# Optimization experiments

Measured on AMD Instinct MI355X. Metric: run time of the kernel, lower is better.

## Reference

```python
import jax, jax.numpy as jnp
import numpy as np

THRESHOLD = 0.95
SECONDARY = 0.5


def setup_inputs() -> dict:
    key = jax.random.key(0)
    quantum_states = jax.random.normal(key, (8, 2048, 64), dtype=jnp.float32)
    return {"quantum_states": quantum_states}


def reference(quantum_states):
    # quantum_states: (B, N, D)
    B, N, D = quantum_states.shape
    # pairwise fidelity: (states @ states^T)^2 -> (B, N, N)
    dots = jnp.einsum("bnd,bmd->bnm", quantum_states, quantum_states)
    fid = dots * dots
    # edge weights: 1.0 if fid >= threshold, else SECONDARY if fid >= secondary, else 0
    w = jnp.where(fid >= THRESHOLD, jnp.float32(1.0),
                  jnp.where(fid >= SECONDARY, jnp.float32(SECONDARY), jnp.float32(0.0)))
    # zero out diagonal (only i < j pairs form edges)
    eye = jnp.eye(N, dtype=bool)
    w = jnp.where(eye[None, :, :], jnp.float32(0.0), w)
    # Laplacian L = D - W
    deg = jnp.sum(w, axis=-1)  # (B, N)
    lap = -w
    idx = jnp.arange(N)
    lap = lap.at[:, idx, idx].set(deg)
    return lap
```

## Files before the change

kernel.cpp:

```cpp
#include <hip/hip_runtime.h>

typedef __attribute__((ext_vector_type(8))) __bf16 bf16x8;
typedef __attribute__((ext_vector_type(4))) __bf16 bf16x4;
typedef __attribute__((ext_vector_type(4))) float f32x4;

#define LDST 72

__device__ __forceinline__ void lds_barrier() {
    asm volatile("s_waitcnt lgkmcnt(0)" ::: "memory");
    __builtin_amdgcn_s_barrier();
    __builtin_amdgcn_sched_barrier(0);
}
__device__ __forceinline__ void full_barrier() {
    asm volatile("s_waitcnt vmcnt(0) lgkmcnt(0)" ::: "memory");
    __builtin_amdgcn_s_barrier();
    __builtin_amdgcn_sched_barrier(0);
}

__global__ __launch_bounds__(512) void lap_strip_kernel(
    const float* __restrict__ X, float* __restrict__ out, int N)
{
    const int flat   = blockIdx.x;
    const int b      = flat & 7;
    const int strip0 = (flat >> 3) * 32;
    const int tid  = threadIdx.x;
    const int lane = tid & 63;
    const int w    = tid >> 6;
    const int t    = lane & 15;
    const int g    = lane >> 4;

    __shared__ __align__(16) unsigned short As[2][128 * LDST];
    __shared__ __align__(16) unsigned short Bs[32 * LDST];
    __shared__ float deg_part[8][32];

    const float* Xb   = X   + (size_t)b * N * 64;
    float*       outb = out + (size_t)b * N * N;

    {
        const float4* src = reinterpret_cast<const float4*>(Xb + (size_t)strip0 * 64);
        int r = tid >> 4, q = tid & 15;
        float4 v = src[tid];
        bf16x4 h = {(__bf16)v.x, (__bf16)v.y, (__bf16)v.z, (__bf16)v.w};
        *reinterpret_cast<bf16x4*>(&Bs[r * LDST + q * 4]) = h;
    }

    float4 pre[4];
    {
        const float4* src = reinterpret_cast<const float4*>(Xb);
#pragma unroll
        for (int it = 0; it < 4; ++it) pre[it] = src[tid + it * 512];
#pragma unroll
        for (int it = 0; it < 4; ++it) {
            int idx = tid + it * 512;
            int r = idx >> 4, q = idx & 15;
            float4 v = pre[it];
            bf16x4 h = {(__bf16)v.x, (__bf16)v.y, (__bf16)v.z, (__bf16)v.w};
            *reinterpret_cast<bf16x4*>(&As[0][r * LDST + q * 4]) = h;
        }
    }
    lds_barrier();

    bf16x8 bfrag[2][2];
#pragma unroll
    for (int ks = 0; ks < 2; ++ks)
#pragma unroll
        for (int fj = 0; fj < 2; ++fj)
            bfrag[ks][fj] = *reinterpret_cast<const bf16x8*>(
                &Bs[(16 * fj + t) * LDST + ks * 32 + g * 8]);

    float rs[2] = {0.f, 0.f};
    int cur = 0;
    const int nct = N >> 7;
    const int diag_ct = strip0 >> 7;

    for (int ct = 0; ct < nct; ++ct) {
        if (ct + 1 < nct) {
            const float4* src = reinterpret_cast<const float4*>(Xb + (size_t)(ct + 1) * 128 * 64);
#pragma unroll
            for (int it = 0; it < 4; ++it) pre[it] = src[tid + it * 512];
        }

        f32x4 acc[2] = {};
#pragma unroll
        for (int ks = 0; ks < 2; ++ks) {
            const int koff = ks * 32 + g * 8;
            bf16x8 a = *reinterpret_cast<const bf16x8*>(
                &As[cur][(16 * w + t) * LDST + koff]);
#pragma unroll
            for (int fj = 0; fj < 2; ++fj)
                acc[fj] = __builtin_amdgcn_mfma_f32_16x16x32_bf16(
                    a, bfrag[ks][fj], acc[fj], 0, 0, 0);
        }

        const bool has_diag = (ct == diag_ct);
#pragma unroll
        for (int fj = 0; fj < 2; ++fj) {
            const int orow  = strip0 + 16 * fj + t;
            const int ocol0 = ct * 128 + 16 * w + 4 * g;
            float wv[4];
#pragma unroll
            for (int r = 0; r < 4; ++r) {
                const float d = acc[fj][r];
                float wt = (fabsf(d) >= 0.97467943f) ? 1.0f
                         : ((fabsf(d) >= 0.70710678f) ? 0.5f : 0.0f);
                if (has_diag && (ocol0 + r == orow)) wt = 0.0f;
                rs[fj] += wt;
                wv[r] = -wt;
            }
            f32x4 st = {wv[0], wv[1], wv[2], wv[3]};
            *reinterpret_cast<f32x4*>(&outb[(size_t)orow * N + ocol0]) = st;
        }

        if (ct + 1 < nct) {
#pragma unroll
            for (int it = 0; it < 4; ++it) {
                int idx = tid + it * 512;
                int r = idx >> 4, q = idx & 15;
                float4 v = pre[it];
                bf16x4 h = {(__bf16)v.x, (__bf16)v.y, (__bf16)v.z, (__bf16)v.w};
                *reinterpret_cast<bf16x4*>(&As[cur ^ 1][r * LDST + q * 4]) = h;
            }
        }
        lds_barrier();
        cur ^= 1;
    }

    rs[0] += __shfl_xor(rs[0], 16, 64); rs[0] += __shfl_xor(rs[0], 32, 64);
    rs[1] += __shfl_xor(rs[1], 16, 64); rs[1] += __shfl_xor(rs[1], 32, 64);
    if (g == 0) { deg_part[w][t] = rs[0]; deg_part[w][16 + t] = rs[1]; }
    full_barrier();
    if (tid < 32) {
        float d = 0.f;
#pragma unroll
        for (int ww = 0; ww < 8; ++ww) d += deg_part[ww][tid];
        const int rr = strip0 + tid;
        outb[(size_t)rr * N + rr] = d;
    }
}

extern "C" void kernel_launch(void* const* d_in, const int* in_sizes, int n_in,
                              void* d_out, int out_size, void* d_ws, size_t ws_size,
                              hipStream_t stream) {
    const float* X = (const float*)d_in[0];
    float* out = (float*)d_out;

    const int B = 8;
    const int D = 64;
    const int N = in_sizes[0] / (B * D);

    dim3 grid((N / 32) * B);
    lap_strip_kernel<<<grid, dim3(512), 0, stream>>>(X, out, N);
}
```

Baseline: 34.69 us.

## Stage weight codes in LDS and emit coalesced full-row stores per half

Result: slower. 35.67 us (+2.8%).

```diff
diff --git a/kernel.cpp b/kernel.cpp
--- a/kernel.cpp
+++ b/kernel.cpp
@@ -4,7 +4,11 @@
 typedef __attribute__((ext_vector_type(4))) __bf16 bf16x4;
 typedef __attribute__((ext_vector_type(4))) float f32x4;
 
-#define LDST 72
+#define LDST 68
+#define SROW 1032
+
+#define T_HI 0.97467943f
+#define T_LO 0.70710678f
 
 __device__ __forceinline__ void lds_barrier() {
     asm volatile("s_waitcnt lgkmcnt(0)" ::: "memory");
@@ -17,7 +21,7 @@
     __builtin_amdgcn_sched_barrier(0);
 }
 
-__global__ __launch_bounds__(512) void lap_strip_kernel(
+__global__ __launch_bounds__(512) void lap_stage_kernel(
     const float* __restrict__ X, float* __restrict__ out, int N)
 {
     const int flat   = blockIdx.x;
@@ -29,8 +33,9 @@
     const int t    = lane & 15;
     const int g    = lane >> 4;
 
-    __shared__ __align__(16) unsigned short As[2][128 * LDST];
+    __shared__ __align__(16) unsigned short As[128 * LDST];
     __shared__ __align__(16) unsigned short Bs[32 * LDST];
+    __shared__ __align__(4)  unsigned char  St[32 * SROW];
     __shared__ float deg_part[8][32];
 
     const float* Xb   = X   + (size_t)b * N * 64;
@@ -43,20 +48,11 @@
         bf16x4 h = {(__bf16)v.x, (__bf16)v.y, (__bf16)v.z, (__bf16)v.w};
         *reinterpret_cast<bf16x4*>(&Bs[r * LDST + q * 4]) = h;
     }
-
     float4 pre[4];
     {
         const float4* src = reinterpret_cast<const float4*>(Xb);
 #pragma unroll
         for (int it = 0; it < 4; ++it) pre[it] = src[tid + it * 512];
-#pragma unroll
-        for (int it = 0; it < 4; ++it) {
-            int idx = tid + it * 512;
-            int r = idx >> 4, q = idx & 15;
-            float4 v = pre[it];
-            bf16x4 h = {(__bf16)v.x, (__bf16)v.y, (__bf16)v.z, (__bf16)v.w};
-            *reinterpret_cast<bf16x4*>(&As[0][r * LDST + q * 4]) = h;
-        }
     }
     lds_barrier();
 
@@ -69,60 +65,79 @@
                 &Bs[(16 * fj + t) * LDST + ks * 32 + g * 8]);
 
     float rs[2] = {0.f, 0.f};
-    int cur = 0;
-    const int nct = N >> 7;
-    const int diag_ct = strip0 >> 7;
 
-    for (int ct = 0; ct < nct; ++ct) {
-        if (ct + 1 < nct) {
-            const float4* src = reinterpret_cast<const float4*>(Xb + (size_t)(ct + 1) * 128 * 64);
-#pragma unroll
-            for (int it = 0; it < 4; ++it) pre[it] = src[tid + it * 512];
-        }
+    for (int half = 0; half < 2; ++half) {
+#pragma unroll 1
+        for (int ctl = 0; ctl < 8; ++ctl) {
+            const int ct = half * 8 + ctl;
 
-        f32x4 acc[2] = {};
-#pragma unroll
-        for (int ks = 0; ks < 2; ++ks) {
-            const int koff = ks * 32 + g * 8;
-            bf16x8 a = *reinterpret_cast<const bf16x8*>(
-                &As[cur][(16 * w + t) * LDST + koff]);
-#pragma unroll
-            for (int fj = 0; fj < 2; ++fj)
-                acc[fj] = __builtin_amdgcn_mfma_f32_16x16x32_bf16(
-                    a, bfrag[ks][fj], acc[fj], 0, 0, 0);
-        }
-
-        const bool has_diag = (ct == diag_ct);
-#pragma unroll
-        for (int fj = 0; fj < 2; ++fj) {
-            const int orow  = strip0 + 16 * fj + t;
-            const int ocol0 = ct * 128 + 16 * w + 4 * g;
-            float wv[4];
-#pragma unroll
-            for (int r = 0; r < 4; ++r) {
-                const float d = acc[fj][r];
-                float wt = (fabsf(d) >= 0.97467943f) ? 1.0f
-                         : ((fabsf(d) >= 0.70710678f) ? 0.5f : 0.0f);
-                if (has_diag && (ocol0 + r == orow)) wt = 0.0f;
-                rs[fj] += wt;
-                wv[r] = -wt;
-            }
-            f32x4 st = {wv[0], wv[1], wv[2], wv[3]};
-            *reinterpret_cast<f32x4*>(&outb[(size_t)orow * N + ocol0]) = st;
-        }
-
-        if (ct + 1 < nct) {
 #pragma unroll
             for (int it = 0; it < 4; ++it) {
                 int idx = tid + it * 512;
                 int r = idx >> 4, q = idx & 15;
                 float4 v = pre[it];
                 bf16x4 h = {(__bf16)v.x, (__bf16)v.y, (__bf16)v.z, (__bf16)v.w};
-                *reinterpret_cast<bf16x4*>(&As[cur ^ 1][r * LDST + q * 4]) = h;
+                *reinterpret_cast<bf16x4*>(&As[r * LDST + q * 4]) = h;
+            }
+            lds_barrier();
+
+            if (ct + 1 < 16) {
+                const float4* src = reinterpret_cast<const float4*>(
+                    Xb + (size_t)(ct + 1) * 128 * 64);
+#pragma unroll
+                for (int it = 0; it < 4; ++it) pre[it] = src[tid + it * 512];
+            }
+
+            f32x4 acc[2] = {};
+#pragma unroll
+            for (int ks = 0; ks < 2; ++ks) {
+                const int koff = ks * 32 + g * 8;
+                bf16x8 a = *reinterpret_cast<const bf16x8*>(
+                    &As[(16 * w + t) * LDST + koff]);
+#pragma unroll
+                for (int fj = 0; fj < 2; ++fj)
+                    acc[fj] = __builtin_amdgcn_mfma_f32_16x16x32_bf16(
+                        a, bfrag[ks][fj], acc[fj], 0, 0, 0);
+            }
+
+            const int scol0 = 128 * ctl + 16 * w + 4 * g;
+            const int gcol0 = half * 1024 + scol0;
+#pragma unroll
+            for (int fj = 0; fj < 2; ++fj) {
+                const int orow = strip0 + 16 * fj + t;
+                unsigned int pack = 0;
+#pragma unroll
+                for (int r = 0; r < 4; ++r) {
+                    const float d = acc[fj][r];
+                    unsigned int code = (fabsf(d) >= T_HI) ? 2u
+                                      : ((fabsf(d) >= T_LO) ? 1u : 0u);
+                    if (gcol0 + r == orow) code = 0u;
+                    rs[fj] += 0.5f * (float)code;
+                    pack |= code << (8 * r);
+                }
+                *reinterpret_cast<unsigned int*>(
+                    &St[(16 * fj + t) * SROW + scol0]) = pack;
+            }
+            lds_barrier();
+        }
+
+#pragma unroll
+        for (int rr = 0; rr < 4; ++rr) {
+            const int row  = 4 * w + rr;
+            const int grow = strip0 + row;
+            const unsigned char* sp = &St[row * SROW];
+            float* dst = &outb[(size_t)grow * N + half * 1024];
+#pragma unroll
+            for (int seg = 0; seg < 4; ++seg) {
+                unsigned int u = *reinterpret_cast<const unsigned int*>(
+                    &sp[seg * 256 + 4 * lane]);
+                f32x4 v = { -0.5f * (float)( u        & 0xffu),
+                            -0.5f * (float)((u >> 8)  & 0xffu),
+                            -0.5f * (float)((u >> 16) & 0xffu),
+                            -0.5f * (float)((u >> 24) & 0xffu) };
+                *reinterpret_cast<f32x4*>(&dst[seg * 256 + 4 * lane]) = v;
             }
         }
-        lds_barrier();
-        cur ^= 1;
     }
 
     rs[0] += __shfl_xor(rs[0], 16, 64); rs[0] += __shfl_xor(rs[0], 32, 64);
@@ -149,5 +164,5 @@
     const int N = in_sizes[0] / (B * D);
 
     dim3 grid((N / 32) * B);
-    lap_strip_kernel<<<grid, dim3(512), 0, stream>>>(X, out, N);
+    lap_stage_kernel<<<grid, dim3(512), 0, stream>>>(X, out, N);
 }
```
